# Kernel tuning notes

Hardware: AMD Instinct MI355X
Metric: run time of the kernel (lower is better)

## Reference

```python
import jax, jax.numpy as jnp
import numpy as np

# RT-DETR deformable attention config
B, Q, D = 32, 300, 256
H, DH = 8, 32          # n_heads, d_head
L, P = 4, 4            # n_levels, n_points
SHAPES = [(80, 80), (40, 40), (20, 20), (10, 10)]
STARTS = [0, 6400, 8000, 8400]
S = 8500               # sum of H_l*W_l


def setup_inputs() -> dict:
    key = jax.random.key(0)
    ks = jax.random.split(key, 8)
    sc = 1.0 / np.sqrt(D)
    return {
        "hidden_states": jax.random.normal(ks[0], (B, Q, D), jnp.float32),
        "encoder_hidden_states": jax.random.normal(ks[1], (B, S, D), jnp.float32),
        "reference_points": jax.random.uniform(ks[2], (B, Q, 1, 4), jnp.float32),
        "W_val": jax.random.normal(ks[3], (D, D), jnp.float32) * sc,
        "b_val": jnp.zeros((D,), jnp.float32),
        "W_off": jax.random.normal(ks[4], (D, H * L * P * 2), jnp.float32) * sc,
        "b_off": jnp.zeros((H * L * P * 2,), jnp.float32),
        "W_attn": jax.random.normal(ks[5], (D, H * L * P), jnp.float32) * sc,
        "b_attn": jnp.zeros((H * L * P,), jnp.float32),
        "W_out": jax.random.normal(ks[6], (D, D), jnp.float32) * sc,
        "b_out": jnp.zeros((D,), jnp.float32),
    }


def _bilinear_sample(v, grid, hh, ww):
    """GridSample, bilinear, align_corners=False, padding_mode='zeros'.

    v:    (N, C, hh*ww) flattened feature map
    grid: (N, Q, P, 2) normalized coords in [-1, 1], (x, y)
    returns (N, C, Q, P)
    """
    gx, gy = grid[..., 0], grid[..., 1]
    # align_corners=False pixel mapping
    x = ((gx + 1.0) * ww - 1.0) * 0.5
    y = ((gy + 1.0) * hh - 1.0) * 0.5
    x0f = jnp.floor(x)
    y0f = jnp.floor(y)
    lx = x - x0f
    ly = y - y0f
    x0 = x0f.astype(jnp.int32)
    y0 = y0f.astype(jnp.int32)
    x1 = x0 + 1
    y1 = y0 + 1

    def gather(xi, yi):
        valid = (xi >= 0) & (xi < ww) & (yi >= 0) & (yi < hh)  # (N,Q,P)
        idx = jnp.clip(yi, 0, hh - 1) * ww + jnp.clip(xi, 0, ww - 1)
        vals = jax.vmap(lambda vb, ib: vb[:, ib])(v, idx)  # (N,C,Q,P)
        return vals * valid[:, None, :, :].astype(v.dtype)

    w00 = ((1.0 - lx) * (1.0 - ly))[:, None]
    w01 = (lx * (1.0 - ly))[:, None]
    w10 = ((1.0 - lx) * ly)[:, None]
    w11 = (lx * ly)[:, None]
    return (gather(x0, y0) * w00 + gather(x1, y0) * w01
            + gather(x0, y1) * w10 + gather(x1, y1) * w11)


def reference(hidden_states, encoder_hidden_states, reference_points,
              W_val, b_val, W_off, b_off, W_attn, b_attn, W_out, b_out):
    # value projection -> (B, S, H, DH)
    value = (encoder_hidden_states @ W_val + b_val).reshape(B, S, H, DH)
    # sampling offsets -> (B, Q, H, L, P, 2)
    off = (hidden_states @ W_off + b_off).reshape(B, Q, H, L, P, 2)
    # attention weights, softmax over L*P jointly per head
    aw = (hidden_states @ W_attn + b_attn).reshape(B, Q, H, L * P)
    aw = jax.nn.softmax(aw, axis=-1).reshape(B, Q, H, L, P)
    # reference box -> broadcastable (B, Q, 1, 1, 1, 2)
    ref_xy = reference_points[:, :, :, :2][:, :, :, None, None, :]
    ref_wh = reference_points[:, :, :, 2:][:, :, :, None, None, :]
    locs = ref_xy + (off / float(P)) * (ref_wh * 0.5)
    grids = 2.0 * locs - 1.0  # (B, Q, H, L, P, 2)

    # fold heads into batch: grid (B*H, Q, L, P, 2), value (B*H, DH, S)
    g = grids.transpose(0, 2, 1, 3, 4, 5).reshape(B * H, Q, L, P, 2)
    v = value.transpose(0, 2, 3, 1).reshape(B * H, DH, S)

    sampled = []
    for lvl, (hh, ww) in enumerate(SHAPES):
        st = STARTS[lvl]
        vl = v[:, :, st:st + hh * ww]          # (B*H, DH, hh*ww)
        gl = g[:, :, lvl]                      # (B*H, Q, P, 2)
        sampled.append(_bilinear_sample(vl, gl, hh, ww))  # (B*H, DH, Q, P)
    out = jnp.stack(sampled, axis=3)           # (B*H, DH, Q, L, P)

    w = aw.transpose(0, 2, 1, 3, 4).reshape(B * H, 1, Q, L, P)
    out = (out * w).sum(axis=(3, 4))           # (B*H, DH, Q)
    out = out.reshape(B, H * DH, Q).transpose(0, 2, 1)  # (B, Q, D)
    return out @ W_out + b_out
```

## Files before the change

kernel.cpp:

```cpp
#include <hip/hip_runtime.h>
#include <hip/hip_bf16.h>

#define BB 32
#define QQ 300
#define DD 256
#define HH 8
#define DHH 32
#define LL 4
#define PP 4
#define SS 8500

typedef __attribute__((ext_vector_type(8))) short bf16x8;
typedef __attribute__((ext_vector_type(8))) _Float16 f16x8;
typedef __attribute__((ext_vector_type(4))) float f32x4;

__device__ inline unsigned short f2bf(float f) {
  unsigned int u = __builtin_bit_cast(unsigned int, f);
  unsigned int r = (u + 0x7FFFu + ((u >> 16) & 1u)) >> 16;
  return (unsigned short)r;
}
__device__ inline unsigned short f2h(float f) {
  return __builtin_bit_cast(unsigned short, (_Float16)f);
}
__device__ inline float h2f(unsigned short u) {
  return (float)__builtin_bit_cast(_Float16, u);
}

__global__ __launch_bounds__(256) void wcvt_kernel(const float* __restrict__ W,
                                                   unsigned short* __restrict__ dst) {
  int t = blockIdx.x * 256 + threadIdx.x;
  int k = t >> 8, n = t & 255;
  dst[n * 256 + (k ^ ((n & 7) << 3))] = f2bf(W[(size_t)k * 256 + n]);
}

template <int N>
__global__ __launch_bounds__(256) void wextf16_kernel(const float* __restrict__ W,
                                                      unsigned short* __restrict__ dst) {
  __shared__ float s_w[64][65];
  constexpr int NT = N / 64;
  const int kt = blockIdx.x / NT;
  const int nt = blockIdx.x % NT;
  const int t = threadIdx.x;
#pragma unroll
  for (int i = 0; i < 16; ++i) {
    int idx = i * 256 + t;
    int kk = idx >> 6, nn = idx & 63;
    s_w[kk][nn] = W[(size_t)(kt * 64 + kk) * N + nt * 64 + nn];
  }
  __syncthreads();
#pragma unroll
  for (int i = 0; i < 16; ++i) {
    int idx = i * 256 + t;
    int nn = idx >> 6, kk = idx & 63;
    const int n = nt * 64 + nn;
    const float v = s_w[kk][nn];
    const unsigned short hi = f2h(v);
    const unsigned short lo = f2h(v - h2f(hi));
    const int ksw = kt * 64 + (kk ^ ((n & 7) << 3));
    dst[(size_t)n * 512 + ksw] = hi;
    dst[(size_t)n * 512 + 256 + ksw] = lo;
  }
}

__global__ __launch_bounds__(256) void hidh_kernel(const float* __restrict__ hidden,
                                                   unsigned short* __restrict__ hidh) {
  int t = blockIdx.x * 256 + threadIdx.x;
  int m = t >> 6, j = (t & 63) * 4;
  float4 v = *reinterpret_cast<const float4*>(hidden + (size_t)m * 256 + j);
  ushort4 h;
  h.x = f2h(v.x); h.y = f2h(v.y); h.z = f2h(v.z); h.w = f2h(v.w);
  *reinterpret_cast<ushort4*>(hidh + (size_t)m * 256 + (j ^ ((m & 7) << 3))) = h;
}

__global__ __launch_bounds__(256, 4) void gemm_val_mfma(
    const float* __restrict__ A, const unsigned short* __restrict__ WbfS,
    const float* __restrict__ bias, __hip_bfloat16* __restrict__ C) {
  __shared__ __align__(16) unsigned short Alds[64 * 64];
  __shared__ __align__(16) unsigned short Blds[256 * 64];

  const int t = threadIdx.x;
  const int lane = t & 63;
  const int w = t >> 6;
  const int lm = lane & 15, lg = lane >> 4;
  const int row0 = blockIdx.x * 64;

  f32x4 acc[16];
#pragma unroll
  for (int nf = 0; nf < 16; ++nf) acc[nf] = {0.f, 0.f, 0.f, 0.f};

  for (int k0 = 0; k0 < 256; k0 += 64) {
#pragma unroll
    for (int i = 0; i < 8; ++i) {
      const unsigned short* gp = WbfS +
          (size_t)(w * 64 + i * 8 + (lane >> 3)) * 256 + k0 + (lane & 7) * 8;
      unsigned char* lp = reinterpret_cast<unsigned char*>(Blds) + (w * 8 + i) * 1024;
      __builtin_amdgcn_global_load_lds(
          (const __attribute__((address_space(1))) void*)gp,
          (__attribute__((address_space(3))) void*)lp, 16, 0, 0);
    }
#pragma unroll
    for (int i = 0; i < 4; ++i) {
      int u = i * 256 + t;
      int r = u >> 4, c4 = (u & 15) * 4;
      float4 v = *reinterpret_cast<const float4*>(A + (size_t)(row0 + r) * 256 + k0 + c4);
      ushort4 h;
      h.x = f2bf(v.x); h.y = f2bf(v.y); h.z = f2bf(v.z); h.w = f2bf(v.w);
      *reinterpret_cast<ushort4*>(&Alds[r * 64 + (c4 ^ ((r & 7) << 3))]) = h;
    }
    __syncthreads();

#pragma unroll
    for (int ks = 0; ks < 2; ++ks) {
      const int kk = (ks * 32 + lg * 8) ^ ((lm & 7) << 3);
      const bf16x8 af = *reinterpret_cast<const bf16x8*>(&Alds[(w * 16 + lm) * 64 + kk]);
#pragma unroll
      for (int nf = 0; nf < 16; ++nf) {
        const bf16x8 bfr = *reinterpret_cast<const bf16x8*>(&Blds[(nf * 16 + lm) * 64 + kk]);
        acc[nf] = __builtin_amdgcn_mfma_f32_16x16x32_bf16(af, bfr, acc[nf], 0, 0, 0);
      }
    }
    __syncthreads();
  }

  const int rb = row0 + w * 16 + lg * 4;
#pragma unroll
  for (int nf = 0; nf < 16; ++nf) {
    const int col = nf * 16 + lm;
    const float bv = bias[col];
#pragma unroll
    for (int j = 0; j < 4; ++j)
      C[(size_t)(rb + j) * 256 + col] = __float2bfloat16(acc[nf][j] + bv);
  }
}

template <int KB, int KA, int N, bool F16>
__global__ __launch_bounds__(256) void gemm_tpl(
    const unsigned short* __restrict__ A, const unsigned short* __restrict__ B,
    const float* __restrict__ bias, float* __restrict__ C) {
  __shared__ __align__(16) unsigned short Alds[64 * 64];
  __shared__ __align__(16) unsigned short Blds[N * 64];

  const int t = threadIdx.x;
  const int lane = t & 63;
  const int w = t >> 6;
  const int lm = lane & 15, lg = lane >> 4;
  const int row0 = blockIdx.x * 64;
  constexpr int NF = N / 16;

  f32x4 acc[NF];
#pragma unroll
  for (int nf = 0; nf < NF; ++nf) acc[nf] = {0.f, 0.f, 0.f, 0.f};

  for (int k0 = 0; k0 < KB; k0 += 64) {
    const int ka = k0 & (KA - 1);
#pragma unroll
    for (int i = 0; i < N / 32; ++i) {
      const int c = w * (N / 32) + i;
      const unsigned short* gp = B + (size_t)(c * 8 + (lane >> 3)) * KB + k0 + (lane & 7) * 8;
      unsigned char* lp = reinterpret_cast<unsigned char*>(Blds) + c * 1024;
      __builtin_amdgcn_global_load_lds(
          (const __attribute__((address_space(1))) void*)gp,
          (__attribute__((address_space(3))) void*)lp, 16, 0, 0);
    }
#pragma unroll
    for (int i = 0; i < 2; ++i) {
      const int c = w * 2 + i;
      const unsigned short* gp = A + (size_t)(row0 + c * 8 + (lane >> 3)) * KA + ka + (lane & 7) * 8;
      unsigned char* lp = reinterpret_cast<unsigned char*>(Alds) + c * 1024;
      __builtin_amdgcn_global_load_lds(
          (const __attribute__((address_space(1))) void*)gp,
          (__attribute__((address_space(3))) void*)lp, 16, 0, 0);
    }
    __syncthreads();

#pragma unroll
    for (int ks = 0; ks < 2; ++ks) {
      const int kk = (ks * 32 + lg * 8) ^ ((lm & 7) << 3);
      const bf16x8 af = *reinterpret_cast<const bf16x8*>(&Alds[(w * 16 + lm) * 64 + kk]);
#pragma unroll
      for (int nf = 0; nf < NF; ++nf) {
        const bf16x8 bfr = *reinterpret_cast<const bf16x8*>(&Blds[(nf * 16 + lm) * 64 + kk]);
        if constexpr (F16)
          acc[nf] = __builtin_amdgcn_mfma_f32_16x16x32_f16(
              __builtin_bit_cast(f16x8, af), __builtin_bit_cast(f16x8, bfr), acc[nf], 0, 0, 0);
        else
          acc[nf] = __builtin_amdgcn_mfma_f32_16x16x32_bf16(af, bfr, acc[nf], 0, 0, 0);
      }
    }
    __syncthreads();
  }

  const int rb = row0 + w * 16 + lg * 4;
#pragma unroll
  for (int nf = 0; nf < NF; ++nf) {
    const int col = nf * 16 + lm;
    const float bv = bias[col];
#pragma unroll
    for (int j = 0; j < 4; ++j)
      C[(size_t)(rb + j) * N + col] = acc[nf][j] + bv;
  }
}

#define QPB 8

__global__ __launch_bounds__(256) void sample_kernel(
    const __hip_bfloat16* __restrict__ value, const float* __restrict__ offb,
    const float* __restrict__ logits, const float* __restrict__ refpts,
    unsigned short* __restrict__ samp) {
  __shared__ float s_off[QPB][256];
  __shared__ float s_lg[QPB][128];

  const int nb = gridDim.x;
  const int bswz = (blockIdx.x % 8) * (nb / 8) + blockIdx.x / 8;
  const int bq0 = bswz * QPB;
  const int t = threadIdx.x;

#pragma unroll
  for (int i = 0; i < QPB; ++i) {
    int idx = i * 256 + t;
    int q = idx >> 8, col = idx & 255;
    s_off[q][col ^ (((col >> 5) & 7) << 2)] = offb[(size_t)bq0 * 256 + idx];
  }
#pragma unroll
  for (int i = 0; i < QPB / 2; ++i) {
    int idx = i * 256 + t;
    s_lg[idx >> 7][idx & 127] = logits[(size_t)bq0 * 128 + idx];
  }
  __syncthreads();

  if (t < QPB * HH) {
    const int q = t >> 3, h = t & 7;
    float* lg = &s_lg[q][h * 16];
    float m = lg[0];
#pragma unroll
    for (int j = 1; j < 16; ++j) m = fmaxf(m, lg[j]);
    float e[16], s = 0.f;
#pragma unroll
    for (int j = 0; j < 16; ++j) { e[j] = __expf(lg[j] - m); s += e[j]; }
    const float inv = 1.f / s;
#pragma unroll
    for (int j = 0; j < 16; ++j) lg[j] = e[j] * inv;
  }
  __syncthreads();

  const int q = t >> 5;
  const int sub = t & 31;
  const int h = sub >> 2;
  const int c4 = sub & 3;
  const int bq = bq0 + q;
  const int b = bq / QQ;

  const float4 ref = *reinterpret_cast<const float4*>(refpts + (size_t)bq * 4);
  const float rx = ref.x, ry = ref.y, rw = ref.z, rh = ref.w;
  const unsigned short* vb =
      (const unsigned short*)value + (size_t)b * SS * DD + h * DHH + c4 * 8;

  float acc[8];
#pragma unroll
  for (int j = 0; j < 8; ++j) acc[j] = 0.f;

  const int dims[4] = {80, 40, 20, 10};
  const int sts[4] = {0, 6400, 8000, 8400};
  const int hsw = h << 2;

#pragma unroll
  for (int l = 0; l < LL; ++l) {
    const int dim = dims[l];
    const int st = sts[l];
    const float fdim = (float)dim;
#pragma unroll
    for (int p = 0; p < PP; ++p) {
      const int tapi = l * 4 + p;
      const float2 oxy =
          *reinterpret_cast<const float2*>(&s_off[q][(h * 32 + 2 * tapi) ^ hsw]);
      const float locx = rx + oxy.x * rw * 0.125f;
      const float locy = ry + oxy.y * rh * 0.125f;
      const float x = locx * fdim - 0.5f;
      const float y = locy * fdim - 0.5f;
      const float x0f = floorf(x), y0f = floorf(y);
      const float fx = x - x0f, fy = y - y0f;
      const int x0 = (int)x0f, y0 = (int)y0f;
      const float wt = s_lg[q][h * 16 + tapi];
      const float bw[4] = {(1.f - fx) * (1.f - fy), fx * (1.f - fy),
                           (1.f - fx) * fy, fx * fy};
      const int cx[4] = {x0, x0 + 1, x0, x0 + 1};
      const int cy[4] = {y0, y0, y0 + 1, y0 + 1};
#pragma unroll
      for (int c = 0; c < 4; ++c) {
        const int xi = cx[c], yi = cy[c];
        const bool valid = (xi >= 0) & (xi < dim) & (yi >= 0) & (yi < dim);
        const int xc = min(max(xi, 0), dim - 1);
        const int yc = min(max(yi, 0), dim - 1);
        const uint4 v = *reinterpret_cast<const uint4*>(
            vb + (size_t)(st + yc * dim + xc) * DD);
        const float wv = valid ? bw[c] * wt : 0.f;
        const unsigned u[4] = {v.x, v.y, v.z, v.w};
#pragma unroll
        for (int k = 0; k < 4; ++k) {
          const float lo = __builtin_bit_cast(float, u[k] << 16);
          const float hi = __builtin_bit_cast(float, u[k] & 0xFFFF0000u);
          acc[2 * k] += lo * wv;
          acc[2 * k + 1] += hi * wv;
        }
      }
    }
  }

  bf16x8 o;
#pragma unroll
  for (int j = 0; j < 8; ++j) o[j] = (short)f2bf(acc[j]);
  const int col = (h * DHH + c4 * 8) ^ ((bq & 7) << 3);
  *reinterpret_cast<bf16x8*>(samp + (size_t)bq * 256 + col) = o;
}

extern "C" void kernel_launch(void* const* d_in, const int* in_sizes, int n_in,
                              void* d_out, int out_size, void* d_ws, size_t ws_size,
                              hipStream_t stream) {
  const float* hidden = (const float*)d_in[0];
  const float* ehs    = (const float*)d_in[1];
  const float* refpts = (const float*)d_in[2];
  const float* W_val  = (const float*)d_in[3];
  const float* b_val  = (const float*)d_in[4];
  const float* W_off  = (const float*)d_in[5];
  const float* b_off  = (const float*)d_in[6];
  const float* W_attn = (const float*)d_in[7];
  const float* b_attn = (const float*)d_in[8];
  const float* W_out  = (const float*)d_in[9];
  const float* b_out  = (const float*)d_in[10];
  float* out = (float*)d_out;

  char* ws = (char*)d_ws;
  __hip_bfloat16* value  = (__hip_bfloat16*)ws;
  unsigned short* wvalS  = (unsigned short*)(ws + 139264000);
  unsigned short* woutS  = (unsigned short*)(ws + 139395072);
  unsigned short* woffE  = (unsigned short*)(ws + 139526144);
  unsigned short* wattE  = (unsigned short*)(ws + 139788288);
  unsigned short* hidh   = (unsigned short*)(ws + 139919360);
  float*          offb   = (float*)(ws + 144834560);
  float*          logitsb= (float*)(ws + 154664960);
  unsigned short* samp   = (unsigned short*)(ws + 159580160);

  const int M_val = BB * SS;
  const int M_q   = BB * QQ;

  wcvt_kernel<<<256, 256, 0, stream>>>(W_val, wvalS);
  wcvt_kernel<<<256, 256, 0, stream>>>(W_out, woutS);
  wextf16_kernel<256><<<16, 256, 0, stream>>>(W_off, woffE);
  wextf16_kernel<128><<<8, 256, 0, stream>>>(W_attn, wattE);
  hidh_kernel<<<M_q * 64 / 256, 256, 0, stream>>>(hidden, hidh);
  gemm_val_mfma<<<M_val / 64, 256, 0, stream>>>(ehs, wvalS, b_val, value);
  gemm_tpl<512, 256, 256, true><<<M_q / 64, 256, 0, stream>>>(hidh, woffE, b_off, offb);
  gemm_tpl<512, 256, 128, true><<<M_q / 64, 256, 0, stream>>>(hidh, wattE, b_attn, logitsb);
  sample_kernel<<<M_q / QPB, 256, 0, stream>>>(value, offb, logitsb, refpts, samp);
  gemm_tpl<256, 256, 256, false><<<M_q / 64, 256, 0, stream>>>(samp, woutS, b_out, out);
}
```

Before: 195.8 us.

## Merge prep kernels into one launch and split sampling levels across two thread halves

Five small weight/hidden conversion kernels are folded into one prep_kernel that dispatches on block index, cutting launch overhead. The sampling kernel now uses 512 threads per block: one half handles levels 0-1 and the other levels 2-3, and their partial sums are combined through shared memory before the bf16 store. This doubles the threads working on each query to expose more memory-level parallelism for the gathers. The cost is an extra shared buffer, a block-wide barrier, and an uneven split since levels 0-1 hold most of the feature map.

```diff
diff --git a/kernel.cpp b/kernel.cpp
--- a/kernel.cpp
+++ b/kernel.cpp
@@ -26,50 +26,58 @@
   return (float)__builtin_bit_cast(_Float16, u);
 }
 
-__global__ __launch_bounds__(256) void wcvt_kernel(const float* __restrict__ W,
-                                                   unsigned short* __restrict__ dst) {
-  int t = blockIdx.x * 256 + threadIdx.x;
-  int k = t >> 8, n = t & 255;
-  dst[n * 256 + (k ^ ((n & 7) << 3))] = f2bf(W[(size_t)k * 256 + n]);
-}
-
-template <int N>
-__global__ __launch_bounds__(256) void wextf16_kernel(const float* __restrict__ W,
-                                                      unsigned short* __restrict__ dst) {
+__global__ __launch_bounds__(256) void prep_kernel(
+    const float* __restrict__ W_val, const float* __restrict__ W_out,
+    const float* __restrict__ W_off, const float* __restrict__ W_attn,
+    const float* __restrict__ hidden,
+    unsigned short* __restrict__ wvalS, unsigned short* __restrict__ woutS,
+    unsigned short* __restrict__ woffE, unsigned short* __restrict__ wattE,
+    unsigned short* __restrict__ hidh) {
   __shared__ float s_w[64][65];
-  constexpr int NT = N / 64;
-  const int kt = blockIdx.x / NT;
-  const int nt = blockIdx.x % NT;
-  const int t = threadIdx.x;
-#pragma unroll
-  for (int i = 0; i < 16; ++i) {
-    int idx = i * 256 + t;
-    int kk = idx >> 6, nn = idx & 63;
-    s_w[kk][nn] = W[(size_t)(kt * 64 + kk) * N + nt * 64 + nn];
-  }
-  __syncthreads();
-#pragma unroll
-  for (int i = 0; i < 16; ++i) {
-    int idx = i * 256 + t;
-    int nn = idx >> 6, kk = idx & 63;
-    const int n = nt * 64 + nn;
-    const float v = s_w[kk][nn];
-    const unsigned short hi = f2h(v);
-    const unsigned short lo = f2h(v - h2f(hi));
-    const int ksw = kt * 64 + (kk ^ ((n & 7) << 3));
-    dst[(size_t)n * 512 + ksw] = hi;
-    dst[(size_t)n * 512 + 256 + ksw] = lo;
-  }
-}
-
-__global__ __launch_bounds__(256) void hidh_kernel(const float* __restrict__ hidden,
-                                                   unsigned short* __restrict__ hidh) {
-  int t = blockIdx.x * 256 + threadIdx.x;
-  int m = t >> 6, j = (t & 63) * 4;
-  float4 v = *reinterpret_cast<const float4*>(hidden + (size_t)m * 256 + j);
-  ushort4 h;
-  h.x = f2h(v.x); h.y = f2h(v.y); h.z = f2h(v.z); h.w = f2h(v.w);
-  *reinterpret_cast<ushort4*>(hidh + (size_t)m * 256 + (j ^ ((m & 7) << 3))) = h;
+  const int blk = blockIdx.x;
+  const int tid = threadIdx.x;
+
+  if (blk < 512) {
+    const float* W = blk < 256 ? W_val : W_out;
+    unsigned short* dst = blk < 256 ? wvalS : woutS;
+    int t = (blk & 255) * 256 + tid;
+    int k = t >> 8, n = t & 255;
+    dst[n * 256 + (k ^ ((n & 7) << 3))] = f2bf(W[(size_t)k * 256 + n]);
+  } else if (blk < 536) {
+    const bool isOff = blk < 528;
+    const int N = isOff ? 256 : 128;
+    const int NT = N / 64;
+    const int lb = isOff ? blk - 512 : blk - 528;
+    const float* W = isOff ? W_off : W_attn;
+    unsigned short* dst = isOff ? woffE : wattE;
+    const int kt = lb / NT, nt = lb % NT;
+#pragma unroll
+    for (int i = 0; i < 16; ++i) {
+      int idx = i * 256 + tid;
+      int kk = idx >> 6, nn = idx & 63;
+      s_w[kk][nn] = W[(size_t)(kt * 64 + kk) * N + nt * 64 + nn];
+    }
+    __syncthreads();
+#pragma unroll
+    for (int i = 0; i < 16; ++i) {
+      int idx = i * 256 + tid;
+      int nn = idx >> 6, kk = idx & 63;
+      const int n = nt * 64 + nn;
+      const float v = s_w[kk][nn];
+      const unsigned short hi = f2h(v);
+      const unsigned short lo = f2h(v - h2f(hi));
+      const int ksw = kt * 64 + (kk ^ ((n & 7) << 3));
+      dst[(size_t)n * 512 + ksw] = hi;
+      dst[(size_t)n * 512 + 256 + ksw] = lo;
+    }
+  } else {
+    int t = (blk - 536) * 256 + tid;
+    int m = t >> 6, j = (t & 63) * 4;
+    float4 v = *reinterpret_cast<const float4*>(hidden + (size_t)m * 256 + j);
+    ushort4 h;
+    h.x = f2h(v.x); h.y = f2h(v.y); h.z = f2h(v.z); h.w = f2h(v.w);
+    *reinterpret_cast<ushort4*>(hidh + (size_t)m * 256 + (j ^ ((m & 7) << 3))) = h;
+  }
 }
 
 __global__ __launch_bounds__(256, 4) void gemm_val_mfma(
@@ -203,12 +211,13 @@
 
 #define QPB 8
 
-__global__ __launch_bounds__(256) void sample_kernel(
+__global__ __launch_bounds__(512) void sample_kernel(
     const __hip_bfloat16* __restrict__ value, const float* __restrict__ offb,
     const float* __restrict__ logits, const float* __restrict__ refpts,
     unsigned short* __restrict__ samp) {
   __shared__ float s_off[QPB][256];
   __shared__ float s_lg[QPB][128];
+  __shared__ float s_part[QPB][256];
 
   const int nb = gridDim.x;
   const int bswz = (blockIdx.x % 8) * (nb / 8) + blockIdx.x / 8;
@@ -216,14 +225,14 @@
   const int t = threadIdx.x;
 
 #pragma unroll
-  for (int i = 0; i < QPB; ++i) {
-    int idx = i * 256 + t;
+  for (int i = 0; i < QPB * 256 / 512; ++i) {
+    int idx = i * 512 + t;
     int q = idx >> 8, col = idx & 255;
     s_off[q][col ^ (((col >> 5) & 7) << 2)] = offb[(size_t)bq0 * 256 + idx];
   }
 #pragma unroll
-  for (int i = 0; i < QPB / 2; ++i) {
-    int idx = i * 256 + t;
+  for (int i = 0; i < QPB * 128 / 512; ++i) {
+    int idx = i * 512 + t;
     s_lg[idx >> 7][idx & 127] = logits[(size_t)bq0 * 128 + idx];
   }
   __syncthreads();
@@ -243,7 +252,8 @@
   }
   __syncthreads();
 
-  const int q = t >> 5;
+  const int q = t >> 6;
+  const int half = (t >> 5) & 1;
   const int sub = t & 31;
   const int h = sub >> 2;
   const int c4 = sub & 3;
@@ -259,14 +269,13 @@
 #pragma unroll
   for (int j = 0; j < 8; ++j) acc[j] = 0.f;
 
-  const int dims[4] = {80, 40, 20, 10};
-  const int sts[4] = {0, 6400, 8000, 8400};
   const int hsw = h << 2;
 
 #pragma unroll
-  for (int l = 0; l < LL; ++l) {
-    const int dim = dims[l];
-    const int st = sts[l];
+  for (int li = 0; li < 2; ++li) {
+    const int dim = half ? (li ? 10 : 20) : (li ? 40 : 80);
+    const int st = half ? (li ? 8400 : 8000) : (li ? 6400 : 0);
+    const int l = half * 2 + li;
     const float fdim = (float)dim;
 #pragma unroll
     for (int p = 0; p < PP; ++p) {
@@ -306,11 +315,21 @@
     }
   }
 
-  bf16x8 o;
-#pragma unroll
-  for (int j = 0; j < 8; ++j) o[j] = (short)f2bf(acc[j]);
-  const int col = (h * DHH + c4 * 8) ^ ((bq & 7) << 3);
-  *reinterpret_cast<bf16x8*>(samp + (size_t)bq * 256 + col) = o;
+  if (half == 1) {
+    *reinterpret_cast<float4*>(&s_part[q][h * DHH + c4 * 8]) =
+        make_float4(acc[0], acc[1], acc[2], acc[3]);
+    *reinterpret_cast<float4*>(&s_part[q][h * DHH + c4 * 8 + 4]) =
+        make_float4(acc[4], acc[5], acc[6], acc[7]);
+  }
+  __syncthreads();
+  if (half == 0) {
+    const float* pp = &s_part[q][h * DHH + c4 * 8];
+    bf16x8 o;
+#pragma unroll
+    for (int j = 0; j < 8; ++j) o[j] = (short)f2bf(acc[j] + pp[j]);
+    const int col = (h * DHH + c4 * 8) ^ ((bq & 7) << 3);
+    *reinterpret_cast<bf16x8*>(samp + (size_t)bq * 256 + col) = o;
+  }
 }
 
 extern "C" void kernel_launch(void* const* d_in, const int* in_sizes, int n_in,
@@ -343,14 +362,11 @@
   const int M_val = BB * SS;
   const int M_q   = BB * QQ;
 
-  wcvt_kernel<<<256, 256, 0, stream>>>(W_val, wvalS);
-  wcvt_kernel<<<256, 256, 0, stream>>>(W_out, woutS);
-  wextf16_kernel<256><<<16, 256, 0, stream>>>(W_off, woffE);
-  wextf16_kernel<128><<<8, 256, 0, stream>>>(W_attn, wattE);
-  hidh_kernel<<<M_q * 64 / 256, 256, 0, stream>>>(hidden, hidh);
+  prep_kernel<<<2936, 256, 0, stream>>>(W_val, W_out, W_off, W_attn, hidden,
+                                        wvalS, woutS, woffE, wattE, hidh);
   gemm_val_mfma<<<M_val / 64, 256, 0, stream>>>(ehs, wvalS, b_val, value);
   gemm_tpl<512, 256, 256, true><<<M_q / 64, 256, 0, stream>>>(hidh, woffE, b_off, offb);
   gemm_tpl<512, 256, 128, true><<<M_q / 64, 256, 0, stream>>>(hidh, wattE, b_attn, logitsb);
-  sample_kernel<<<M_q / QPB, 256, 0, stream>>>(value, offb, logitsb, refpts, samp);
+  sample_kernel<<<M_q / QPB, 512, 0, stream>>>(value, offb, logitsb, refpts, samp);
   gemm_tpl<256, 256, 256, false><<<M_q / 64, 256, 0, stream>>>(samp, woutS, b_out, out);
 }
```

Result: no change. 194.6 us (-0.6%).
